# Optimization experiments

Hardware: AMD Instinct MI355X
Metric: run time of the kernel (lower is better)

Reference implementation:

```python
import jax, jax.numpy as jnp
import numpy as np

NUM_NODES = 100000
NUM_EDGES = 625000
IN_FEATURES = 128
OUT_FEATURES = 128


def setup_inputs() -> dict:
    key = jax.random.key(0)
    k1, k2, k3, k4 = jax.random.split(key, 4)
    x = jax.random.normal(k1, (NUM_NODES, IN_FEATURES), dtype=jnp.float32)
    edge_index = jax.random.randint(k2, (2, NUM_EDGES), 0, NUM_NODES, dtype=jnp.int64)
    # Xavier uniform for W (fan_in=IN, fan_out=OUT); B initialized to zeros in the
    # original, but we use small random values so gradients flow through both paths.
    limit = float(np.sqrt(6.0 / (IN_FEATURES + OUT_FEATURES)))
    W = jax.random.uniform(k3, (OUT_FEATURES, IN_FEATURES), dtype=jnp.float32,
                           minval=-limit, maxval=limit)
    B = jax.random.uniform(k4, (OUT_FEATURES, IN_FEATURES), dtype=jnp.float32,
                           minval=-limit, maxval=limit)
    return {"x": x, "edge_index": edge_index, "W": W, "B": B}


def reference(x, edge_index, W, B):
    sources, destinations = edge_index[0], edge_index[1]
    # message: gather destination features, scatter-add into source slots
    messages = x[destinations]                                        # [E, F_in]
    agg = jax.ops.segment_sum(messages, sources, num_segments=x.shape[0])  # [N, F_in]
    # in-degree (w.r.t. sources) normalization; zero-degree -> divide by 1
    deg = jax.ops.segment_sum(jnp.ones((sources.shape[0],), dtype=x.dtype),
                              sources, num_segments=x.shape[0])       # [N]
    deg = jnp.where(deg == 0, jnp.ones_like(deg), deg)
    agg = agg / deg[:, None]
    # update: (W @ messages.T + B @ x.T).T == messages @ W.T + x @ B.T
    out = agg @ W.T + x @ B.T                                         # [N, F_out]
    return out
```

## Files before the change

kernel.cpp:

```cpp
#include <hip/hip_runtime.h>

#define F_IN   128
#define F_OUT  128

typedef __attribute__((ext_vector_type(8))) short short8;
typedef __attribute__((ext_vector_type(4))) float floatx4;

__device__ __forceinline__ float bf16u_to_f_lo(unsigned int u) {
    union { unsigned int i; float f; } c; c.i = u << 16; return c.f;
}
__device__ __forceinline__ float bf16u_to_f_hi(unsigned int u) {
    union { unsigned int i; float f; } c; c.i = u & 0xffff0000u; return c.f;
}
__device__ __forceinline__ unsigned short f_to_bf16(float f) {
    union { float f; unsigned int i; } c; c.f = f;
    unsigned int u = c.i;
    u += 0x7fffu + ((u >> 16) & 1u);
    return (unsigned short)(u >> 16);
}
__device__ __forceinline__ unsigned int pack2(unsigned short a, unsigned short b) {
    return (unsigned int)a | ((unsigned int)b << 16);
}

__device__ __forceinline__ void gload_lds16(const void* g, void* l) {
    __builtin_amdgcn_global_load_lds(
        (const __attribute__((address_space(1))) unsigned int*)g,
        (__attribute__((address_space(3))) unsigned int*)l, 16, 0, 0);
}

__global__ __launch_bounds__(256) void init_kernel(const float* __restrict__ x,
                                                   char* __restrict__ outb,
                                                   const float* __restrict__ W,
                                                   const float* __restrict__ Bm,
                                                   uint4* __restrict__ bfrag,
                                                   int* __restrict__ btot,
                                                   const int* __restrict__ ei,
                                                   int N, int E, int nbconv, int nbhist) {
    int b = blockIdx.x;
    int t = threadIdx.x;
    if (b < nbconv) {
        long tid = (long)b * 256 + t;
        if (tid < (long)N * 32) {
            int row = (int)(tid >> 5);
            int seg = (int)(tid & 31);
            float4 v = *(const float4*)(x + (size_t)row * 128 + seg * 4);
            unsigned short r[4] = {f_to_bf16(v.x), f_to_bf16(v.y), f_to_bf16(v.z), f_to_bf16(v.w)};
            *(ushort4*)(outb + (size_t)row * 512 + 256 + seg * 8) =
                make_ushort4(r[0], r[1], r[2], r[3]);
        }
        return;
    }
    if (b < nbconv + nbhist) {
        __shared__ int h[256];
        h[t] = 0;
        __syncthreads();
        int e0 = (b - nbconv) * 1024;
#pragma unroll
        for (int j = 0; j < 4; ++j) {
            int idx = e0 + j * 256 + t;
            if (idx < E) atomicAdd(&h[ei[idx] >> 9], 1);
        }
        __syncthreads();
        if (h[t]) atomicAdd(&btot[t], h[t]);
        return;
    }
#pragma unroll
    for (int i = 0; i < 16; ++i) {
        int flat = i * 256 + t;
        int lane = flat & 63;
        int idx = flat >> 6;
        int nt = idx >> 3, sfrag = idx & 7;
        int n = nt * 16 + (lane & 15);
        int kbase = sfrag * 32 + (lane >> 4) * 8;
        const float* srcp = (kbase < 128) ? (W + n * 128 + kbase)
                                          : (Bm + n * 128 + (kbase - 128));
        float4 v0 = *(const float4*)srcp;
        float4 v1 = *(const float4*)(srcp + 4);
        uint4 pk;
        pk.x = pack2(f_to_bf16(v0.x), f_to_bf16(v0.y));
        pk.y = pack2(f_to_bf16(v0.z), f_to_bf16(v0.w));
        pk.z = pack2(f_to_bf16(v1.x), f_to_bf16(v1.y));
        pk.w = pack2(f_to_bf16(v1.z), f_to_bf16(v1.w));
        bfrag[flat] = pk;
    }
}

__global__ __launch_bounds__(256) void scan256_kernel(const int* __restrict__ btot,
                                                      int* __restrict__ gbase,
                                                      int* __restrict__ gcur, int NB) {
    __shared__ int s[256];
    int t = threadIdx.x;
    s[t] = (t < NB) ? btot[t] : 0;
    __syncthreads();
    for (int d = 1; d < 256; d <<= 1) {
        int v = s[t] + ((t >= d) ? s[t - d] : 0);
        __syncthreads();
        s[t] = v;
        __syncthreads();
    }
    int excl = (t > 0) ? s[t - 1] : 0;
    if (t < NB) { gbase[t] = excl; gcur[t] = excl; }
    if (t == 0) gbase[NB] = s[255];
}

__global__ __launch_bounds__(256) void pass1_kernel(const int* __restrict__ ei,
                                                    int* __restrict__ gcur,
                                                    int* __restrict__ ebuf, int E) {
    __shared__ int cnt[256];
    __shared__ int base[256];
    __shared__ int cur[256];
    int t = threadIdx.x;
    cnt[t] = 0;
    cur[t] = 0;
    int e0 = blockIdx.x * 1024;
    __syncthreads();
    int s[4];
#pragma unroll
    for (int j = 0; j < 4; ++j) {
        int idx = e0 + j * 256 + t;
        s[j] = (idx < E) ? ei[idx] : -1;
        if (s[j] >= 0) atomicAdd(&cnt[s[j] >> 9], 1);
    }
    __syncthreads();
    int c = cnt[t];
    base[t] = c ? atomicAdd(&gcur[t], c) : 0;
    __syncthreads();
#pragma unroll
    for (int j = 0; j < 4; ++j) {
        if (s[j] >= 0) {
            int idx = e0 + j * 256 + t;
            int bkt = s[j] >> 9;
            int r = atomicAdd(&cur[bkt], 1);
            int d = ei[E + idx];
            ebuf[base[bkt] + r] = ((s[j] & 511) << 17) | d;
        }
    }
}

__global__ __launch_bounds__(256) void pass2_kernel(const int* __restrict__ ebuf,
                                                    const int* __restrict__ gbase,
                                                    int* __restrict__ off,
                                                    int* __restrict__ dst_sorted,
                                                    int N, int NB) {
    __shared__ int sc[512];
    __shared__ int cur[512];
    int g = blockIdx.x, t = threadIdx.x;
    int lo = g << 9;
    int hi = min(N, lo + 512);
    int start = gbase[g];
    int end = gbase[g + 1];
    sc[t] = 0;
    sc[t + 256] = 0;
    __syncthreads();
    for (int i = start + t; i < end; i += 256) atomicAdd(&sc[ebuf[i] >> 17], 1);
    __syncthreads();
    for (int d = 1; d < 512; d <<= 1) {
        int v0 = sc[t] + ((t >= d) ? sc[t - d] : 0);
        int i1 = t + 256;
        int v1 = sc[i1] + sc[i1 - d];
        __syncthreads();
        sc[t] = v0;
        sc[i1] = v1;
        __syncthreads();
    }
    if (lo + t < hi) off[lo + t] = start + sc[t];
    cur[t] = (t == 0) ? 0 : sc[t - 1];
    {
        int i1 = t + 256;
        if (lo + i1 < hi) off[lo + i1] = start + sc[i1];
        cur[i1] = sc[i1 - 1];
    }
    __syncthreads();
    for (int i = start + t; i < end; i += 256) {
        int v = ebuf[i];
        int n = v >> 17;
        int r = atomicAdd(&cur[n], 1);
        dst_sorted[start + r] = v & 0x1FFFF;
    }
}

__global__ __launch_bounds__(256) void gather_bf16_kernel(const int* __restrict__ off,
                                                          const int* __restrict__ dst_sorted,
                                                          char* __restrict__ outb, int N) {
    int node = blockIdx.x * 16 + (threadIdx.x >> 4);
    int lane = threadIdx.x & 15;
    if (node >= N) return;
    int start = (node == 0) ? 0 : off[node - 1];
    int end = off[node];
    float acc[8];
#pragma unroll
    for (int i = 0; i < 8; ++i) acc[i] = 0.0f;

    const char* xb = outb;
    int j = start;
    for (; j + 4 <= end; j += 4) {
        int d0 = dst_sorted[j];
        int d1 = dst_sorted[j + 1];
        int d2 = dst_sorted[j + 2];
        int d3 = dst_sorted[j + 3];
        uint4 a = *(const uint4*)(xb + (size_t)d0 * 512 + 256 + lane * 16);
        uint4 b = *(const uint4*)(xb + (size_t)d1 * 512 + 256 + lane * 16);
        uint4 c = *(const uint4*)(xb + (size_t)d2 * 512 + 256 + lane * 16);
        uint4 d = *(const uint4*)(xb + (size_t)d3 * 512 + 256 + lane * 16);
        acc[0] += bf16u_to_f_lo(a.x); acc[1] += bf16u_to_f_hi(a.x);
        acc[2] += bf16u_to_f_lo(a.y); acc[3] += bf16u_to_f_hi(a.y);
        acc[4] += bf16u_to_f_lo(a.z); acc[5] += bf16u_to_f_hi(a.z);
        acc[6] += bf16u_to_f_lo(a.w); acc[7] += bf16u_to_f_hi(a.w);
        acc[0] += bf16u_to_f_lo(b.x); acc[1] += bf16u_to_f_hi(b.x);
        acc[2] += bf16u_to_f_lo(b.y); acc[3] += bf16u_to_f_hi(b.y);
        acc[4] += bf16u_to_f_lo(b.z); acc[5] += bf16u_to_f_hi(b.z);
        acc[6] += bf16u_to_f_lo(b.w); acc[7] += bf16u_to_f_hi(b.w);
        acc[0] += bf16u_to_f_lo(c.x); acc[1] += bf16u_to_f_hi(c.x);
        acc[2] += bf16u_to_f_lo(c.y); acc[3] += bf16u_to_f_hi(c.y);
        acc[4] += bf16u_to_f_lo(c.z); acc[5] += bf16u_to_f_hi(c.z);
        acc[6] += bf16u_to_f_lo(c.w); acc[7] += bf16u_to_f_hi(c.w);
        acc[0] += bf16u_to_f_lo(d.x); acc[1] += bf16u_to_f_hi(d.x);
        acc[2] += bf16u_to_f_lo(d.y); acc[3] += bf16u_to_f_hi(d.y);
        acc[4] += bf16u_to_f_lo(d.z); acc[5] += bf16u_to_f_hi(d.z);
        acc[6] += bf16u_to_f_lo(d.w); acc[7] += bf16u_to_f_hi(d.w);
    }
    for (; j < end; ++j) {
        int d0 = dst_sorted[j];
        uint4 a = *(const uint4*)(xb + (size_t)d0 * 512 + 256 + lane * 16);
        acc[0] += bf16u_to_f_lo(a.x); acc[1] += bf16u_to_f_hi(a.x);
        acc[2] += bf16u_to_f_lo(a.y); acc[3] += bf16u_to_f_hi(a.y);
        acc[4] += bf16u_to_f_lo(a.z); acc[5] += bf16u_to_f_hi(a.z);
        acc[6] += bf16u_to_f_lo(a.w); acc[7] += bf16u_to_f_hi(a.w);
    }
    int deg = end - start;
    float scale = (deg > 0) ? (1.0f / (float)deg) : 1.0f;
    unsigned short r[8];
#pragma unroll
    for (int i = 0; i < 8; ++i) r[i] = f_to_bf16(acc[i] * scale);
    uint4 pk;
    pk.x = pack2(r[0], r[1]);
    pk.y = pack2(r[2], r[3]);
    pk.z = pack2(r[4], r[5]);
    pk.w = pack2(r[6], r[7]);
    *(uint4*)(outb + (size_t)node * 512 + lane * 16) = pk;
}

__global__ __launch_bounds__(256, 2) void gemm_mfma_kernel(const uint4* __restrict__ bfrag,
                                                           float* __restrict__ out, int N) {
    __shared__ uint4 Bs[4096];
    int t = threadIdx.x;
    int lane = t & 63;
    int w = t >> 6;
    int m16 = lane & 15;
    int quad = lane >> 4;

#pragma unroll
    for (int j = 0; j < 16; ++j)
        gload_lds16(bfrag + (w * 16 + j) * 64 + lane, &Bs[(w * 16 + j) * 64]);

    int rowbase = blockIdx.x * 128 + w * 32;
    short8 afrag[2][8];
#pragma unroll
    for (int g = 0; g < 2; ++g) {
        int arow = rowbase + g * 16 + m16;
        if (arow > N - 1) arow = N - 1;
        const char* ab = (const char*)out + (size_t)arow * 512;
#pragma unroll
        for (int s = 0; s < 8; ++s)
            afrag[g][s] = *(const short8*)(ab + s * 64 + quad * 16);
    }
    __syncthreads();

    floatx4 acc[2][8];
#pragma unroll
    for (int g = 0; g < 2; ++g)
#pragma unroll
        for (int nt = 0; nt < 8; ++nt) acc[g][nt] = (floatx4){0.f, 0.f, 0.f, 0.f};

#pragma unroll
    for (int nt = 0; nt < 8; ++nt) {
#pragma unroll
        for (int s = 0; s < 8; ++s) {
            short8 bf = *(const short8*)&Bs[(nt * 8 + s) * 64 + lane];
            acc[0][nt] = __builtin_amdgcn_mfma_f32_16x16x32_bf16(afrag[0][s], bf, acc[0][nt], 0, 0, 0);
            acc[1][nt] = __builtin_amdgcn_mfma_f32_16x16x32_bf16(afrag[1][s], bf, acc[1][nt], 0, 0, 0);
        }
    }

#pragma unroll
    for (int g = 0; g < 2; ++g)
#pragma unroll
        for (int nt = 0; nt < 8; ++nt)
#pragma unroll
            for (int r = 0; r < 4; ++r) {
                int gr = rowbase + g * 16 + quad * 4 + r;
                if (gr < N) out[(size_t)gr * 128 + nt * 16 + m16] = acc[g][nt][r];
            }
}

__global__ void zero_kernel(int* __restrict__ p, long n) {
    long i = (long)blockIdx.x * blockDim.x + threadIdx.x;
    long stride = (long)gridDim.x * blockDim.x;
    for (; i < n; i += stride) p[i] = 0;
}

__global__ void invdeg_kernel(int* __restrict__ deg_io, int N) {
    int i = blockIdx.x * blockDim.x + threadIdx.x;
    if (i < N) {
        int d = deg_io[i];
        float inv = (d > 0) ? (1.0f / (float)d) : 1.0f;
        ((float*)deg_io)[i] = inv;
    }
}

__global__ void hist_kernel(const int* __restrict__ src, int* __restrict__ cnt, int E) {
    int e = blockIdx.x * blockDim.x + threadIdx.x;
    if (e < E) atomicAdd(&cnt[src[e]], 1);
}

__global__ __launch_bounds__(128) void scatter_atomic_kernel(const float* __restrict__ x,
                                                             const int* __restrict__ ei,
                                                             const float* __restrict__ invdeg,
                                                             float* __restrict__ out, int E) {
    int e = blockIdx.x;
    int f = threadIdx.x;
    int s = ei[e];
    int d = ei[E + e];
    float v = x[(long)d * F_IN + f] * invdeg[s];
    atomicAdd(&out[(long)s * F_IN + f], v);
}

__global__ __launch_bounds__(256) void gemm_fused_kernel(const float* __restrict__ x,
                                                         const float* __restrict__ W,
                                                         const float* __restrict__ Bm,
                                                         float* __restrict__ out, int N) {
    __shared__ float As[64][68];
    __shared__ float Ms[64][132];
    int t = threadIdx.x;
    int row0 = blockIdx.x * 64;
    int c0 = (t & 31) * 4;
    int r0 = (t >> 5) * 8;
    float acc[8][4];
#pragma unroll
    for (int i = 0; i < 8; ++i)
#pragma unroll
        for (int j = 0; j < 4; ++j) acc[i][j] = 0.0f;

    for (int kc = 0; kc < 4; ++kc) {
        const float* Asrc = (kc < 2) ? out : x;
        const float* Msrc = (kc < 2) ? W : Bm;
        int k0 = (kc & 1) * 64;
#pragma unroll
        for (int i = 0; i < 4; ++i) {
            int flat = t + 256 * i;
            int m = flat >> 4, ks = flat & 15;
            int row = row0 + m;
            float4 v = make_float4(0.f, 0.f, 0.f, 0.f);
            if (row < N) v = *(const float4*)&Asrc[(long)row * 128 + k0 + ks * 4];
            As[ks * 4 + 0][m] = v.x;
            As[ks * 4 + 1][m] = v.y;
            As[ks * 4 + 2][m] = v.z;
            As[ks * 4 + 3][m] = v.w;
        }
#pragma unroll
        for (int i = 0; i < 8; ++i) {
            int flat = t + 256 * i;
            int c = flat >> 4, ks = flat & 15;
            float4 v = *(const float4*)&Msrc[(long)c * 128 + k0 + ks * 4];
            Ms[ks * 4 + 0][c] = v.x;
            Ms[ks * 4 + 1][c] = v.y;
            Ms[ks * 4 + 2][c] = v.z;
            Ms[ks * 4 + 3][c] = v.w;
        }
        __syncthreads();
#pragma unroll 8
        for (int kk = 0; kk < 64; ++kk) {
            float4 a0 = *(const float4*)&As[kk][r0];
            float4 a1 = *(const float4*)&As[kk][r0 + 4];
            float4 m0 = *(const float4*)&Ms[kk][c0];
            float a[8] = {a0.x, a0.y, a0.z, a0.w, a1.x, a1.y, a1.z, a1.w};
            float m[4] = {m0.x, m0.y, m0.z, m0.w};
#pragma unroll
            for (int i = 0; i < 8; ++i)
#pragma unroll
                for (int j = 0; j < 4; ++j) acc[i][j] += a[i] * m[j];
        }
        __syncthreads();
    }
#pragma unroll
    for (int i = 0; i < 8; ++i) {
        int row = row0 + r0 + i;
        if (row < N) {
            float4 v = make_float4(acc[i][0], acc[i][1], acc[i][2], acc[i][3]);
            *(float4*)&out[(long)row * 128 + c0] = v;
        }
    }
}


extern "C" void kernel_launch(void* const* d_in, const int* in_sizes, int n_in,
                              void* d_out, int out_size, void* d_ws, size_t ws_size,
                              hipStream_t stream) {
    const float* x = (const float*)d_in[0];
    const int* ei = (const int*)d_in[1];
    const float* W = (const float*)d_in[2];
    const float* Bm = (const float*)d_in[3];
    float* out = (float*)d_out;

    const int N = in_sizes[0] / F_IN;
    const int E = in_sizes[1] / 2;
    const int NB = (N + 511) >> 9;

    const size_t need_main = 4096 * sizeof(uint4) +
                             ((size_t)772 + (size_t)N + 2 * (size_t)E) * sizeof(int);
    const size_t need_deg = (size_t)N * sizeof(int);

    if (ws_size >= need_main && N <= 131072) {
        uint4* bfrag = (uint4*)d_ws;
        int* btot    = (int*)(bfrag + 4096);
        int* gbase   = btot + 256;
        int* gcur    = gbase + 260;
        int* off     = gcur + 256;
        int* ebuf    = off + N;
        int* dst_sorted = ebuf + E;

        const int nbconv = (int)(((long)N * 32 + 255) / 256);
        const int nbhist = (E + 1023) / 1024;

        hipMemsetAsync(btot, 0, 256 * sizeof(int), stream);
        init_kernel<<<nbconv + nbhist + 1, 256, 0, stream>>>(x, (char*)out, W, Bm,
                                                             bfrag, btot, ei, N, E,
                                                             nbconv, nbhist);
        scan256_kernel<<<1, 256, 0, stream>>>(btot, gbase, gcur, NB);
        pass1_kernel<<<(E + 1023) / 1024, 256, 0, stream>>>(ei, gcur, ebuf, E);
        pass2_kernel<<<NB, 256, 0, stream>>>(ebuf, gbase, off, dst_sorted, N, NB);
        gather_bf16_kernel<<<(N + 15) / 16, 256, 0, stream>>>(off, dst_sorted, (char*)out, N);
        gemm_mfma_kernel<<<(N + 127) / 128, 256, 0, stream>>>(bfrag, out, N);
    } else if (ws_size >= need_deg) {
        int* deg = (int*)d_ws;
        zero_kernel<<<256, 256, 0, stream>>>(deg, N);
        hist_kernel<<<(E + 255) / 256, 256, 0, stream>>>(ei, deg, E);
        invdeg_kernel<<<(N + 255) / 256, 256, 0, stream>>>(deg, N);
        zero_kernel<<<512, 256, 0, stream>>>((int*)out, (long)N * F_IN);
        scatter_atomic_kernel<<<E, 128, 0, stream>>>(x, ei, (const float*)deg, out, E);
        gemm_fused_kernel<<<(N + 63) / 64, 256, 0, stream>>>(x, W, Bm, out, N);
    }
}
```

Before: 198.8 us.

## Drop memset via per-block histograms and halve GEMM LDS/registers for occupancy

Histogram blocks now write their per-bucket counts to a dense per-block array instead of atomically adding into a global total. The single-block scan kernel sums these columns, which removes the hipMemsetAsync call and the global atomics. The MFMA GEMM now stages B in two K-halves through a 32KB LDS buffer and holds only half of the A fragments at a time. The smaller LDS and register footprint allows 3 blocks per CU, at the cost of an extra barrier phase and a serial column-sum in the one-block scan.

After: 216.0 us. +8.7%, slower.

```diff
diff --git a/kernel.cpp b/kernel.cpp
--- a/kernel.cpp
+++ b/kernel.cpp
@@ -33,7 +33,7 @@
                                                    const float* __restrict__ W,
                                                    const float* __restrict__ Bm,
                                                    uint4* __restrict__ bfrag,
-                                                   int* __restrict__ btot,
+                                                   int* __restrict__ H,
                                                    const int* __restrict__ ei,
                                                    int N, int E, int nbconv, int nbhist) {
     int b = blockIdx.x;
@@ -61,7 +61,7 @@
             if (idx < E) atomicAdd(&h[ei[idx] >> 9], 1);
         }
         __syncthreads();
-        if (h[t]) atomicAdd(&btot[t], h[t]);
+        H[(size_t)(b - nbconv) * 256 + t] = h[t];
         return;
     }
 #pragma unroll
@@ -85,12 +85,22 @@
     }
 }
 
-__global__ __launch_bounds__(256) void scan256_kernel(const int* __restrict__ btot,
+__global__ __launch_bounds__(256) void scan256_kernel(const int* __restrict__ H,
+                                                      int nbhist,
                                                       int* __restrict__ gbase,
                                                       int* __restrict__ gcur, int NB) {
     __shared__ int s[256];
     int t = threadIdx.x;
-    s[t] = (t < NB) ? btot[t] : 0;
+    int s0 = 0, s1 = 0, s2 = 0, s3 = 0;
+    int i = 0;
+    for (; i + 4 <= nbhist; i += 4) {
+        s0 += H[(size_t)(i + 0) * 256 + t];
+        s1 += H[(size_t)(i + 1) * 256 + t];
+        s2 += H[(size_t)(i + 2) * 256 + t];
+        s3 += H[(size_t)(i + 3) * 256 + t];
+    }
+    for (; i < nbhist; ++i) s0 += H[(size_t)i * 256 + t];
+    s[t] = s0 + s1 + s2 + s3;
     __syncthreads();
     for (int d = 1; d < 256; d <<= 1) {
         int v = s[t] + ((t >= d) ? s[t - d] : 0);
@@ -240,9 +250,9 @@
     *(uint4*)(outb + (size_t)node * 512 + lane * 16) = pk;
 }
 
-__global__ __launch_bounds__(256, 2) void gemm_mfma_kernel(const uint4* __restrict__ bfrag,
+__global__ __launch_bounds__(256, 3) void gemm_mfma_kernel(const uint4* __restrict__ bfrag,
                                                            float* __restrict__ out, int N) {
-    __shared__ uint4 Bs[4096];
+    __shared__ uint4 Bs[2048];
     int t = threadIdx.x;
     int lane = t & 63;
     int w = t >> 6;
@@ -250,21 +260,25 @@
     int quad = lane >> 4;
 
 #pragma unroll
-    for (int j = 0; j < 16; ++j)
-        gload_lds16(bfrag + (w * 16 + j) * 64 + lane, &Bs[(w * 16 + j) * 64]);
+    for (int j = 0; j < 8; ++j) {
+        int r = w * 8 + j;
+        gload_lds16(bfrag + (((r >> 2) * 8 + (r & 3)) * 64 + lane), &Bs[r * 64]);
+    }
 
     int rowbase = blockIdx.x * 128 + w * 32;
-    short8 afrag[2][8];
+    const char* ab[2];
 #pragma unroll
     for (int g = 0; g < 2; ++g) {
         int arow = rowbase + g * 16 + m16;
         if (arow > N - 1) arow = N - 1;
-        const char* ab = (const char*)out + (size_t)arow * 512;
-#pragma unroll
-        for (int s = 0; s < 8; ++s)
-            afrag[g][s] = *(const short8*)(ab + s * 64 + quad * 16);
-    }
-    __syncthreads();
+        ab[g] = (const char*)out + (size_t)arow * 512;
+    }
+    short8 af[2][4];
+#pragma unroll
+    for (int g = 0; g < 2; ++g)
+#pragma unroll
+        for (int sl = 0; sl < 4; ++sl)
+            af[g][sl] = *(const short8*)(ab[g] + sl * 64 + quad * 16);
 
     floatx4 acc[2][8];
 #pragma unroll
@@ -272,15 +286,38 @@
 #pragma unroll
         for (int nt = 0; nt < 8; ++nt) acc[g][nt] = (floatx4){0.f, 0.f, 0.f, 0.f};
 
-#pragma unroll
-    for (int nt = 0; nt < 8; ++nt) {
-#pragma unroll
-        for (int s = 0; s < 8; ++s) {
-            short8 bf = *(const short8*)&Bs[(nt * 8 + s) * 64 + lane];
-            acc[0][nt] = __builtin_amdgcn_mfma_f32_16x16x32_bf16(afrag[0][s], bf, acc[0][nt], 0, 0, 0);
-            acc[1][nt] = __builtin_amdgcn_mfma_f32_16x16x32_bf16(afrag[1][s], bf, acc[1][nt], 0, 0, 0);
-        }
-    }
+    __syncthreads();
+
+#pragma unroll
+    for (int nt = 0; nt < 8; ++nt)
+#pragma unroll
+        for (int sl = 0; sl < 4; ++sl) {
+            short8 bf = *(const short8*)&Bs[(nt * 4 + sl) * 64 + lane];
+            acc[0][nt] = __builtin_amdgcn_mfma_f32_16x16x32_bf16(af[0][sl], bf, acc[0][nt], 0, 0, 0);
+            acc[1][nt] = __builtin_amdgcn_mfma_f32_16x16x32_bf16(af[1][sl], bf, acc[1][nt], 0, 0, 0);
+        }
+    __syncthreads();
+
+#pragma unroll
+    for (int j = 0; j < 8; ++j) {
+        int r = w * 8 + j;
+        gload_lds16(bfrag + (((r >> 2) * 8 + 4 + (r & 3)) * 64 + lane), &Bs[r * 64]);
+    }
+#pragma unroll
+    for (int g = 0; g < 2; ++g)
+#pragma unroll
+        for (int sl = 0; sl < 4; ++sl)
+            af[g][sl] = *(const short8*)(ab[g] + 256 + sl * 64 + quad * 16);
+    __syncthreads();
+
+#pragma unroll
+    for (int nt = 0; nt < 8; ++nt)
+#pragma unroll
+        for (int sl = 0; sl < 4; ++sl) {
+            short8 bf = *(const short8*)&Bs[(nt * 4 + sl) * 64 + lane];
+            acc[0][nt] = __builtin_amdgcn_mfma_f32_16x16x32_bf16(af[0][sl], bf, acc[0][nt], 0, 0, 0);
+            acc[1][nt] = __builtin_amdgcn_mfma_f32_16x16x32_bf16(af[1][sl], bf, acc[1][nt], 0, 0, 0);
+        }
 
 #pragma unroll
     for (int g = 0; g < 2; ++g)
@@ -405,28 +442,26 @@
     const int N = in_sizes[0] / F_IN;
     const int E = in_sizes[1] / 2;
     const int NB = (N + 511) >> 9;
+    const int nbconv = (int)(((long)N * 32 + 255) / 256);
+    const int nbhist = (E + 1023) / 1024;
 
     const size_t need_main = 4096 * sizeof(uint4) +
-                             ((size_t)772 + (size_t)N + 2 * (size_t)E) * sizeof(int);
+                             ((size_t)nbhist * 256 + 516 + (size_t)N + 2 * (size_t)E) * sizeof(int);
     const size_t need_deg = (size_t)N * sizeof(int);
 
     if (ws_size >= need_main && N <= 131072) {
         uint4* bfrag = (uint4*)d_ws;
-        int* btot    = (int*)(bfrag + 4096);
-        int* gbase   = btot + 256;
+        int* H       = (int*)(bfrag + 4096);
+        int* gbase   = H + (size_t)nbhist * 256;
         int* gcur    = gbase + 260;
         int* off     = gcur + 256;
         int* ebuf    = off + N;
         int* dst_sorted = ebuf + E;
 
-        const int nbconv = (int)(((long)N * 32 + 255) / 256);
-        const int nbhist = (E + 1023) / 1024;
-
-        hipMemsetAsync(btot, 0, 256 * sizeof(int), stream);
         init_kernel<<<nbconv + nbhist + 1, 256, 0, stream>>>(x, (char*)out, W, Bm,
-                                                             bfrag, btot, ei, N, E,
+                                                             bfrag, H, ei, N, E,
                                                              nbconv, nbhist);
-        scan256_kernel<<<1, 256, 0, stream>>>(btot, gbase, gcur, NB);
+        scan256_kernel<<<1, 256, 0, stream>>>(H, nbhist, gbase, gcur, NB);
         pass1_kernel<<<(E + 1023) / 1024, 256, 0, stream>>>(ei, gcur, ebuf, E);
         pass2_kernel<<<NB, 256, 0, stream>>>(ebuf, gbase, off, dst_sorted, N, NB);
         gather_bf16_kernel<<<(N + 15) / 16, 256, 0, stream>>>(off, dst_sorted, (char*)out, N);
```
